# Kernel tuning notes

Measured on AMD Instinct MI355X. Metric: run time of the kernel, lower is better.

The kernel has to match this reference:

```python
import jax, jax.numpy as jnp
import numpy as np

HIDDEN = 1024
NUM_EXPERTS = 64
MIN_K, MAX_K = 1, 4
THRESHOLD = 0.5
N_TOKENS = 32768


def setup_inputs() -> dict:
    key = jax.random.key(0)
    ks = jax.random.split(key, 6)
    std = 0.02
    h4 = HIDDEN // 4
    return {
        "hidden_states": jax.random.normal(ks[0], (N_TOKENS, HIDDEN), dtype=jnp.float32),
        "router_w": std * jax.random.normal(ks[1], (NUM_EXPERTS, HIDDEN), dtype=jnp.float32),
        "w1": std * jax.random.normal(ks[2], (h4, HIDDEN), dtype=jnp.float32),
        "b1": jnp.zeros((h4,), dtype=jnp.float32),
        "w2": std * jax.random.normal(ks[3], (1, h4), dtype=jnp.float32),
        "b2": jnp.zeros((1,), dtype=jnp.float32),
    }


def reference(hidden_states, router_w, w1, b1, w2, b2):
    # complexity predictor: Linear -> ReLU -> Linear -> Sigmoid, squeeze(-1)
    h = jax.nn.relu(hidden_states @ w1.T + b1)                     # [N, H/4]
    complexity = jax.nn.sigmoid(h @ w2.T + b2)[:, 0]               # [N]
    router_logits = hidden_states @ router_w.T                     # [N, E]

    adaptive_k = jnp.where(complexity > THRESHOLD, MAX_K, MIN_K)   # [N] int

    # vectorized adaptive top-k: take MAX_K everywhere, mask beyond k
    top_vals, top_idx = jax.lax.top_k(router_logits, MAX_K)        # [N, MAX_K]
    pos_mask = jnp.arange(MAX_K)[None, :] < adaptive_k[:, None]    # [N, MAX_K]
    masked_vals = jnp.where(pos_mask, top_vals, -jnp.inf)
    expert_weights = jax.nn.softmax(masked_vals, axis=-1)
    expert_weights = jnp.where(pos_mask, expert_weights, 0.0)      # zeros past k
    selected_experts = jnp.where(pos_mask, top_idx, 0)             # zeros past k

    # routing statistics
    probs = jax.nn.softmax(router_logits, axis=-1)                 # [N, E]
    expert_load = probs.mean(axis=0)                               # [E]
    load_variance = expert_load.var(ddof=1)                        # torch .var() is unbiased
    entropy = -(probs * jnp.log(probs + 1e-8)).sum(axis=-1).mean()

    return router_logits, selected_experts, expert_weights, load_variance, entropy
```

## Files before the change

### kernel.cpp

```cpp
#include <hip/hip_runtime.h>
#include <hip/hip_bf16.h>
#include <math.h>

#define NTOK 32768
#define HID  1024
#define NEXP 64
#define H4   256

typedef __attribute__((ext_vector_type(8))) short bf16x8;
typedef __attribute__((ext_vector_type(8))) unsigned short u16x8;
typedef __attribute__((ext_vector_type(4))) float f32x4;

static __device__ __forceinline__ ushort f2bf(float x) {
    unsigned u = __float_as_uint(x);
    unsigned r = (u + 0x7FFFu + ((u >> 16) & 1u)) >> 16;
    return (ushort)r;
}

static __device__ __forceinline__ void split3r(float x, ushort &h, ushort &m, ushort &l) {
    h = f2bf(x);
    const float r1 = x - __uint_as_float(((unsigned)h) << 16);
    m = f2bf(r1);
    const float r2 = r1 - __uint_as_float(((unsigned)m) << 16);
    l = f2bf(r2);
}

#define SWZ(row, us) ((us) ^ (((row) & 7) << 3))

__global__ __launch_bounds__(256) void prep_kernel(
    const float* __restrict__ W1, const float* __restrict__ RW,
    ushort* __restrict__ W1f, ushort* __restrict__ RWf)
{
    if (blockIdx.x < 256) {
        const int id = blockIdx.x * 256 + threadIdx.x;
        const int c  = id >> 8;
        const int k0 = (id & 255) * 4;
        const float4 v = *(const float4*)(W1 + (size_t)c * HID + k0);
        const int p = k0 >> 5, quad = (k0 >> 3) & 3, kk = k0 & 7;
        const int cg = c >> 6, j = (c >> 4) & 3, l15 = c & 15;
        const int lane = quad * 16 + l15;
        const size_t base = (size_t)p * 16384 + cg * 4096 + j * 1024 + lane * 8 + kk;
        const float xs[4] = {v.x, v.y, v.z, v.w};
        ushort hv[4], lv[4];
#pragma unroll
        for (int q = 0; q < 4; q++) {
            const ushort h = f2bf(xs[q]);
            hv[q] = h;
            lv[q] = f2bf(xs[q] - __uint_as_float(((unsigned)h) << 16));
        }
        *(ushort4*)(W1f + base)       = make_ushort4(hv[0], hv[1], hv[2], hv[3]);
        *(ushort4*)(W1f + base + 512) = make_ushort4(lv[0], lv[1], lv[2], lv[3]);
    } else {
        const int e  = blockIdx.x - 256;
        const int k0 = threadIdx.x * 4;
        const float4 v = *(const float4*)(RW + (size_t)e * HID + k0);
        const int p = k0 >> 5, quad = (k0 >> 3) & 3, kk = k0 & 7;
        const int cg = e >> 4, l15 = e & 15;
        const int lane = quad * 16 + l15;
        const size_t base = (size_t)p * 6144 + cg * 1536 + lane * 8 + kk;
        const float xs[4] = {v.x, v.y, v.z, v.w};
        ushort h[4], m[4], l[4];
#pragma unroll
        for (int q = 0; q < 4; q++) split3r(xs[q], h[q], m[q], l[q]);
        *(ushort4*)(RWf + base)        = make_ushort4(h[0], h[1], h[2], h[3]);
        *(ushort4*)(RWf + base + 512)  = make_ushort4(m[0], m[1], m[2], m[3]);
        *(ushort4*)(RWf + base + 1024) = make_ushort4(l[0], l[1], l[2], l[3]);
    }
}

template<int PH>
__device__ __forceinline__ void kstep(
    int p, int cg, int lane, int quad, int l15, int row, int kc,
    const float* __restrict__ xsrc,
    const ushort* __restrict__ RWf, const ushort* __restrict__ W1f,
    ushort (&Xh)[2][2048], ushort (&Xm)[2][2048], ushort (&Xl)[2][2048],
    bf16x8 (&rwh)[2], bf16x8 (&rwm)[2], bf16x8 (&rwl)[2],
    float4 (&xp)[2][2],
    f32x4 (&accL)[4], f32x4 (&accP)[4][4])
{
    const ushort* __restrict__ w1p = W1f + (size_t)p * 16384 + cg * 4096 + lane * 8;
    bf16x8 bwh[4], bwl[4];
#pragma unroll
    for (int j = 0; j < 4; ++j) {
        bwh[j] = *(const bf16x8*)(w1p + j * 1024);
        bwl[j] = *(const bf16x8*)(w1p + j * 1024 + 512);
    }
    {
        const ushort* __restrict__ rwp =
            RWf + (size_t)((p + 1) & 31) * 6144 + cg * 1536 + lane * 8;
        rwh[PH ^ 1] = *(const bf16x8*)(rwp);
        rwm[PH ^ 1] = *(const bf16x8*)(rwp + 512);
        rwl[PH ^ 1] = *(const bf16x8*)(rwp + 1024);
    }
    xp[PH ^ 1][0] = *(const float4*)(xsrc + (size_t)((p + 2) & 31) * 32);
    xp[PH ^ 1][1] = *(const float4*)(xsrc + (size_t)((p + 2) & 31) * 32 + 4);

    bf16x8 axh[4], axm[4], axl[4];
#pragma unroll
    for (int f = 0; f < 4; ++f) {
        const int ra = f * 16 + l15;
        const int ua = SWZ(ra, ra * 32 + quad * 8);
        axh[f] = *(const bf16x8*)&Xh[PH][ua];
        axm[f] = *(const bf16x8*)&Xm[PH][ua];
        axl[f] = *(const bf16x8*)&Xl[PH][ua];
    }

    {
        const float xs[8] = {xp[PH][0].x, xp[PH][0].y, xp[PH][0].z, xp[PH][0].w,
                             xp[PH][1].x, xp[PH][1].y, xp[PH][1].z, xp[PH][1].w};
        u16x8 sh, sm, sl;
#pragma unroll
        for (int q = 0; q < 8; ++q) {
            ushort h, m, l;
            split3r(xs[q], h, m, l);
            sh[q] = h; sm[q] = m; sl[q] = l;
        }
        const int us = SWZ(row, row * 32 + kc * 8);
        *(u16x8*)&Xh[PH ^ 1][us] = sh;
        *(u16x8*)&Xm[PH ^ 1][us] = sm;
        *(u16x8*)&Xl[PH ^ 1][us] = sl;
    }

#pragma unroll
    for (int f = 0; f < 4; ++f) {
        accL[f] = __builtin_amdgcn_mfma_f32_16x16x32_bf16(axh[f], rwh[PH], accL[f], 0, 0, 0);
        accL[f] = __builtin_amdgcn_mfma_f32_16x16x32_bf16(axm[f], rwh[PH], accL[f], 0, 0, 0);
        accL[f] = __builtin_amdgcn_mfma_f32_16x16x32_bf16(axh[f], rwm[PH], accL[f], 0, 0, 0);
        accL[f] = __builtin_amdgcn_mfma_f32_16x16x32_bf16(axl[f], rwh[PH], accL[f], 0, 0, 0);
        accL[f] = __builtin_amdgcn_mfma_f32_16x16x32_bf16(axh[f], rwl[PH], accL[f], 0, 0, 0);
        accL[f] = __builtin_amdgcn_mfma_f32_16x16x32_bf16(axm[f], rwm[PH], accL[f], 0, 0, 0);
    }
#pragma unroll
    for (int j = 0; j < 4; ++j)
#pragma unroll
        for (int f = 0; f < 4; ++f) {
            accP[f][j] = __builtin_amdgcn_mfma_f32_16x16x32_bf16(axh[f], bwh[j], accP[f][j], 0, 0, 0);
            accP[f][j] = __builtin_amdgcn_mfma_f32_16x16x32_bf16(axm[f], bwh[j], accP[f][j], 0, 0, 0);
            accP[f][j] = __builtin_amdgcn_mfma_f32_16x16x32_bf16(axh[f], bwl[j], accP[f][j], 0, 0, 0);
        }

    asm volatile("s_waitcnt lgkmcnt(0)" ::: "memory");
    __builtin_amdgcn_s_barrier();
    __builtin_amdgcn_sched_barrier(0);
}

__global__ __launch_bounds__(256, 2) void fused_mfma(
    const float* __restrict__ X,
    const ushort* __restrict__ RWf, const ushort* __restrict__ W1f,
    const float* __restrict__ B1, const float* __restrict__ W2,
    float* __restrict__ logits, float* __restrict__ s2ws)
{
    __shared__ __align__(16) ushort Xh[2][2048], Xm[2][2048], Xl[2][2048];
    __shared__ float red[4][64];

    const int tid  = threadIdx.x;
    const int lane = tid & 63;
    const int cg   = tid >> 6;
    const int quad = lane >> 4, l15 = lane & 15;
    const int tok0 = blockIdx.x * 64;

    const int row = tid >> 2;
    const int kc  = tid & 3;

    f32x4 accL[4];
    f32x4 accP[4][4];
#pragma unroll
    for (int f = 0; f < 4; f++) {
        accL[f] = (f32x4){0.f, 0.f, 0.f, 0.f};
#pragma unroll
        for (int j = 0; j < 4; j++) accP[f][j] = (f32x4){0.f, 0.f, 0.f, 0.f};
    }

    const float* __restrict__ xsrc = X + (size_t)(tok0 + row) * HID + kc * 8;

    bf16x8 rwh[2], rwm[2], rwl[2];
    float4 xp[2][2];

    {
        const float4 a0 = *(const float4*)(xsrc);
        const float4 a1 = *(const float4*)(xsrc + 4);
        const float xs[8] = {a0.x, a0.y, a0.z, a0.w, a1.x, a1.y, a1.z, a1.w};
        u16x8 sh, sm, sl;
#pragma unroll
        for (int q = 0; q < 8; ++q) {
            ushort h, m, l;
            split3r(xs[q], h, m, l);
            sh[q] = h; sm[q] = m; sl[q] = l;
        }
        const int us = SWZ(row, row * 32 + kc * 8);
        *(u16x8*)&Xh[0][us] = sh;
        *(u16x8*)&Xm[0][us] = sm;
        *(u16x8*)&Xl[0][us] = sl;
    }
    {
        const ushort* __restrict__ rwp = RWf + (size_t)cg * 1536 + lane * 8;
        rwh[0] = *(const bf16x8*)(rwp);
        rwm[0] = *(const bf16x8*)(rwp + 512);
        rwl[0] = *(const bf16x8*)(rwp + 1024);
    }
    xp[0][0] = *(const float4*)(xsrc + 32);
    xp[0][1] = *(const float4*)(xsrc + 36);
    __syncthreads();

    for (int p = 0; p < 32; p += 2) {
        kstep<0>(p,     cg, lane, quad, l15, row, kc, xsrc, RWf, W1f,
                 Xh, Xm, Xl, rwh, rwm, rwl, xp, accL, accP);
        kstep<1>(p + 1, cg, lane, quad, l15, row, kc, xsrc, RWf, W1f,
                 Xh, Xm, Xl, rwh, rwm, rwl, xp, accL, accP);
    }

#pragma unroll
    for (int f = 0; f < 4; ++f)
#pragma unroll
        for (int r = 0; r < 4; ++r)
            logits[(size_t)(tok0 + f * 16 + quad * 4 + r) * NEXP
                   + cg * 16 + l15] = accL[f][r];

    float w2r[4], b1r[4];
#pragma unroll
    for (int j = 0; j < 4; ++j) {
        const int col = (cg * 4 + j) * 16 + l15;
        w2r[j] = W2[col];
        b1r[j] = B1[col];
    }
#pragma unroll
    for (int f = 0; f < 4; ++f) {
#pragma unroll
        for (int r = 0; r < 4; ++r) {
            float s = 0.f;
#pragma unroll
            for (int j = 0; j < 4; ++j) {
                const float hval = accP[f][j][r] + b1r[j];
                s = fmaf(w2r[j], fmaxf(hval, 0.f), s);
            }
            s += __shfl_xor(s, 1);
            s += __shfl_xor(s, 2);
            s += __shfl_xor(s, 4);
            s += __shfl_xor(s, 8);
            if (l15 == 0)
                red[cg][f * 16 + quad * 4 + r] = s;
        }
    }
    __syncthreads();
    if (tid < 64)
        s2ws[tok0 + tid] = red[0][tid] + red[1][tid] + red[2][tid] + red[3][tid];
}

__global__ __launch_bounds__(64) void route_kernel(
    const float* __restrict__ logits, const float* __restrict__ s2ws,
    const float* __restrict__ B2, float* __restrict__ sel,
    float* __restrict__ wts, float* __restrict__ load_sum,
    float* __restrict__ ent_sum)
{
    const int lane = threadIdx.x;
    const int tok  = blockIdx.x * 64 + lane;

    float r[64];
    const float* lr = logits + (size_t)tok * NEXP;
#pragma unroll
    for (int e4 = 0; e4 < 16; e4++) {
        float4 v = *(const float4*)(lr + e4 * 4);
        r[e4 * 4 + 0] = v.x; r[e4 * 4 + 1] = v.y;
        r[e4 * 4 + 2] = v.z; r[e4 * 4 + 3] = v.w;
    }

    float v0 = -1e30f, v1 = -1e30f, v2 = -1e30f, v3 = -1e30f;
    int   i0 = 0, i1 = 0, i2 = 0, i3 = 0;
#pragma unroll
    for (int e = 0; e < 64; e++) {
        const float v = r[e];
        if (v > v3) {
            if (v > v2) {
                if (v > v1) {
                    if (v > v0) { v3=v2;i3=i2; v2=v1;i2=i1; v1=v0;i1=i0; v0=v;i0=e; }
                    else        { v3=v2;i3=i2; v2=v1;i2=i1; v1=v;i1=e; }
                } else          { v3=v2;i3=i2; v2=v;i2=e; }
            } else              { v3=v;i3=e; }
        }
    }

    const float s2 = s2ws[tok] + B2[0];
    const bool k4 = (s2 > 0.f);

    float w0, w1v, w2v, w3v;
    int   s1i, s2i, s3i;
    if (k4) {
        const float e0 = expf(v0 - v0), e1 = expf(v1 - v0);
        const float e2 = expf(v2 - v0), e3 = expf(v3 - v0);
        const float inv4 = 1.f / (e0 + e1 + e2 + e3);
        w0 = e0 * inv4; w1v = e1 * inv4; w2v = e2 * inv4; w3v = e3 * inv4;
        s1i = i1; s2i = i2; s3i = i3;
    } else {
        w0 = 1.f; w1v = 0.f; w2v = 0.f; w3v = 0.f;
        s1i = 0; s2i = 0; s3i = 0;
    }
    {
        float4 sv = {(float)i0, (float)s1i, (float)s2i, (float)s3i};
        float4 wv = {w0, w1v, w2v, w3v};
        *(float4*)(sel + (size_t)tok * 4) = sv;
        *(float4*)(wts + (size_t)tok * 4) = wv;
    }

    const float mx = v0;
    float S = 0.f, pz = 0.f;
#pragma unroll
    for (int e = 0; e < 64; e++) {
        const float z = r[e] - mx;
        const float t = expf(z);
        S += t; pz = fmaf(t, z, pz);
        r[e] = t;
    }
    const float inv = 1.f / S;
    float ent = logf(S) - pz * inv;

    float myload = 0.f;
#pragma unroll
    for (int e = 0; e < 64; e++) {
        float s = r[e] * inv;
        s += __shfl_xor(s, 1);
        s += __shfl_xor(s, 2);
        s += __shfl_xor(s, 4);
        s += __shfl_xor(s, 8);
        s += __shfl_xor(s, 16);
        s += __shfl_xor(s, 32);
        if (lane == e) myload = s;
    }
    atomicAdd(&load_sum[lane], myload);

    ent += __shfl_xor(ent, 1);
    ent += __shfl_xor(ent, 2);
    ent += __shfl_xor(ent, 4);
    ent += __shfl_xor(ent, 8);
    ent += __shfl_xor(ent, 16);
    ent += __shfl_xor(ent, 32);
    if (lane == 0) atomicAdd(ent_sum, ent);
}

__global__ void finalize_kernel(const float* __restrict__ load_sum,
                                const float* __restrict__ ent_sum,
                                float* __restrict__ out_scal)
{
    const int lane = threadIdx.x;
    const float le = load_sum[lane] * (1.f / (float)NTOK);
    float s = le;
#pragma unroll
    for (int o = 32; o >= 1; o >>= 1) s += __shfl_xor(s, o);
    const float mean = s * (1.f / 64.f);
    const float d = le - mean;
    float v = d * d;
#pragma unroll
    for (int o = 32; o >= 1; o >>= 1) v += __shfl_xor(v, o);
    if (lane == 0) {
        out_scal[0] = v * (1.f / 63.f);
        out_scal[1] = ent_sum[0] * (1.f / (float)NTOK);
    }
}

extern "C" void kernel_launch(void* const* d_in, const int* in_sizes, int n_in,
                              void* d_out, int out_size, void* d_ws, size_t ws_size,
                              hipStream_t stream) {
    const float* X  = (const float*)d_in[0];
    const float* RW = (const float*)d_in[1];
    const float* W1 = (const float*)d_in[2];
    const float* B1 = (const float*)d_in[3];
    const float* W2 = (const float*)d_in[4];
    const float* B2 = (const float*)d_in[5];

    float* out    = (float*)d_out;
    float* logits = out;
    float* sel    = out + (size_t)NTOK * NEXP;
    float* wts    = sel + (size_t)NTOK * 4;
    float* scal   = wts + (size_t)NTOK * 4;

    float* s2ws     = (float*)d_ws;
    float* load_sum = s2ws + NTOK;
    float* ent_sum  = load_sum + 64;
    ushort* W1f = (ushort*)(s2ws + NTOK + 256);
    ushort* RWf = W1f + (size_t)32 * 16384;

    hipMemsetAsync(load_sum, 0, 65 * sizeof(float), stream);

    prep_kernel<<<320, 256, 0, stream>>>(W1, RW, W1f, RWf);
    fused_mfma<<<NTOK / 64, 256, 0, stream>>>(X, RWf, W1f, B1, W2, logits, s2ws);
    route_kernel<<<NTOK / 64, 64, 0, stream>>>(logits, s2ws, B2, sel, wts, load_sum, ent_sum);
    finalize_kernel<<<1, 64, 0, stream>>>(load_sum, ent_sum, scal);
}
```

Baseline: 281.0 us.

## Fuse routing into MFMA kernel and double-buffer W1 fragment loads

The separate route_kernel is merged into the fused MFMA kernel. Logits are staged in a padded shared tile and one wave does top-k, softmax weights, entropy and load reduction, which removes a global logits re-read, the s2ws round trip and a launch. W1 fragments are now prefetched one k-step ahead into double-buffered registers, so global load latency overlaps the MFMAs. The extra shared memory (about 16.6KB) and the extra VGPRs for double-buffered bwh/bwl may reduce occupancy under launch_bounds(256,2). The routing tail also runs on only one of the four waves per block.

```diff
diff --git a/kernel.cpp b/kernel.cpp
--- a/kernel.cpp
+++ b/kernel.cpp
@@ -75,22 +75,25 @@
     const ushort* __restrict__ RWf, const ushort* __restrict__ W1f,
     ushort (&Xh)[2][2048], ushort (&Xm)[2][2048], ushort (&Xl)[2][2048],
     bf16x8 (&rwh)[2], bf16x8 (&rwm)[2], bf16x8 (&rwl)[2],
+    bf16x8 (&bwh)[2][4], bf16x8 (&bwl)[2][4],
     float4 (&xp)[2][2],
     f32x4 (&accL)[4], f32x4 (&accP)[4][4])
 {
-    const ushort* __restrict__ w1p = W1f + (size_t)p * 16384 + cg * 4096 + lane * 8;
-    bf16x8 bwh[4], bwl[4];
-#pragma unroll
-    for (int j = 0; j < 4; ++j) {
-        bwh[j] = *(const bf16x8*)(w1p + j * 1024);
-        bwl[j] = *(const bf16x8*)(w1p + j * 1024 + 512);
-    }
     {
         const ushort* __restrict__ rwp =
             RWf + (size_t)((p + 1) & 31) * 6144 + cg * 1536 + lane * 8;
         rwh[PH ^ 1] = *(const bf16x8*)(rwp);
         rwm[PH ^ 1] = *(const bf16x8*)(rwp + 512);
         rwl[PH ^ 1] = *(const bf16x8*)(rwp + 1024);
+    }
+    {
+        const ushort* __restrict__ w1p =
+            W1f + (size_t)((p + 1) & 31) * 16384 + cg * 4096 + lane * 8;
+#pragma unroll
+        for (int j = 0; j < 4; ++j) {
+            bwh[PH ^ 1][j] = *(const bf16x8*)(w1p + j * 1024);
+            bwl[PH ^ 1][j] = *(const bf16x8*)(w1p + j * 1024 + 512);
+        }
     }
     xp[PH ^ 1][0] = *(const float4*)(xsrc + (size_t)((p + 2) & 31) * 32);
     xp[PH ^ 1][1] = *(const float4*)(xsrc + (size_t)((p + 2) & 31) * 32 + 4);
@@ -134,9 +137,9 @@
     for (int j = 0; j < 4; ++j)
 #pragma unroll
         for (int f = 0; f < 4; ++f) {
-            accP[f][j] = __builtin_amdgcn_mfma_f32_16x16x32_bf16(axh[f], bwh[j], accP[f][j], 0, 0, 0);
-            accP[f][j] = __builtin_amdgcn_mfma_f32_16x16x32_bf16(axm[f], bwh[j], accP[f][j], 0, 0, 0);
-            accP[f][j] = __builtin_amdgcn_mfma_f32_16x16x32_bf16(axh[f], bwl[j], accP[f][j], 0, 0, 0);
+            accP[f][j] = __builtin_amdgcn_mfma_f32_16x16x32_bf16(axh[f], bwh[PH][j], accP[f][j], 0, 0, 0);
+            accP[f][j] = __builtin_amdgcn_mfma_f32_16x16x32_bf16(axm[f], bwh[PH][j], accP[f][j], 0, 0, 0);
+            accP[f][j] = __builtin_amdgcn_mfma_f32_16x16x32_bf16(axh[f], bwl[PH][j], accP[f][j], 0, 0, 0);
         }
 
     asm volatile("s_waitcnt lgkmcnt(0)" ::: "memory");
@@ -148,10 +151,14 @@
     const float* __restrict__ X,
     const ushort* __restrict__ RWf, const ushort* __restrict__ W1f,
     const float* __restrict__ B1, const float* __restrict__ W2,
-    float* __restrict__ logits, float* __restrict__ s2ws)
+    const float* __restrict__ B2,
+    float* __restrict__ logits, float* __restrict__ sel,
+    float* __restrict__ wts, float* __restrict__ load_sum,
+    float* __restrict__ ent_sum)
 {
     __shared__ __align__(16) ushort Xh[2][2048], Xm[2][2048], Xl[2][2048];
     __shared__ float red[4][64];
+    __shared__ float Lt[64][65];
 
     const int tid  = threadIdx.x;
     const int lane = tid & 63;
@@ -174,6 +181,7 @@
     const float* __restrict__ xsrc = X + (size_t)(tok0 + row) * HID + kc * 8;
 
     bf16x8 rwh[2], rwm[2], rwl[2];
+    bf16x8 bwh[2][4], bwl[2][4];
     float4 xp[2][2];
 
     {
@@ -197,6 +205,12 @@
         rwh[0] = *(const bf16x8*)(rwp);
         rwm[0] = *(const bf16x8*)(rwp + 512);
         rwl[0] = *(const bf16x8*)(rwp + 1024);
+        const ushort* __restrict__ w1p = W1f + (size_t)cg * 4096 + lane * 8;
+#pragma unroll
+        for (int j = 0; j < 4; ++j) {
+            bwh[0][j] = *(const bf16x8*)(w1p + j * 1024);
+            bwl[0][j] = *(const bf16x8*)(w1p + j * 1024 + 512);
+        }
     }
     xp[0][0] = *(const float4*)(xsrc + 32);
     xp[0][1] = *(const float4*)(xsrc + 36);
@@ -204,17 +218,19 @@
 
     for (int p = 0; p < 32; p += 2) {
         kstep<0>(p,     cg, lane, quad, l15, row, kc, xsrc, RWf, W1f,
-                 Xh, Xm, Xl, rwh, rwm, rwl, xp, accL, accP);
+                 Xh, Xm, Xl, rwh, rwm, rwl, bwh, bwl, xp, accL, accP);
         kstep<1>(p + 1, cg, lane, quad, l15, row, kc, xsrc, RWf, W1f,
-                 Xh, Xm, Xl, rwh, rwm, rwl, xp, accL, accP);
+                 Xh, Xm, Xl, rwh, rwm, rwl, bwh, bwl, xp, accL, accP);
     }
 
 #pragma unroll
     for (int f = 0; f < 4; ++f)
 #pragma unroll
-        for (int r = 0; r < 4; ++r)
-            logits[(size_t)(tok0 + f * 16 + quad * 4 + r) * NEXP
-                   + cg * 16 + l15] = accL[f][r];
+        for (int r = 0; r < 4; ++r) {
+            const int trow = f * 16 + quad * 4 + r;
+            logits[(size_t)(tok0 + trow) * NEXP + cg * 16 + l15] = accL[f][r];
+            Lt[trow][cg * 16 + l15] = accL[f][r];
+        }
 
     float w2r[4], b1r[4];
 #pragma unroll
@@ -242,98 +258,86 @@
         }
     }
     __syncthreads();
-    if (tid < 64)
-        s2ws[tok0 + tid] = red[0][tid] + red[1][tid] + red[2][tid] + red[3][tid];
-}
-
-__global__ __launch_bounds__(64) void route_kernel(
-    const float* __restrict__ logits, const float* __restrict__ s2ws,
-    const float* __restrict__ B2, float* __restrict__ sel,
-    float* __restrict__ wts, float* __restrict__ load_sum,
-    float* __restrict__ ent_sum)
-{
-    const int lane = threadIdx.x;
-    const int tok  = blockIdx.x * 64 + lane;
-
-    float r[64];
-    const float* lr = logits + (size_t)tok * NEXP;
-#pragma unroll
-    for (int e4 = 0; e4 < 16; e4++) {
-        float4 v = *(const float4*)(lr + e4 * 4);
-        r[e4 * 4 + 0] = v.x; r[e4 * 4 + 1] = v.y;
-        r[e4 * 4 + 2] = v.z; r[e4 * 4 + 3] = v.w;
-    }
-
-    float v0 = -1e30f, v1 = -1e30f, v2 = -1e30f, v3 = -1e30f;
-    int   i0 = 0, i1 = 0, i2 = 0, i3 = 0;
-#pragma unroll
-    for (int e = 0; e < 64; e++) {
-        const float v = r[e];
-        if (v > v3) {
-            if (v > v2) {
-                if (v > v1) {
-                    if (v > v0) { v3=v2;i3=i2; v2=v1;i2=i1; v1=v0;i1=i0; v0=v;i0=e; }
-                    else        { v3=v2;i3=i2; v2=v1;i2=i1; v1=v;i1=e; }
-                } else          { v3=v2;i3=i2; v2=v;i2=e; }
-            } else              { v3=v;i3=e; }
-        }
-    }
-
-    const float s2 = s2ws[tok] + B2[0];
-    const bool k4 = (s2 > 0.f);
-
-    float w0, w1v, w2v, w3v;
-    int   s1i, s2i, s3i;
-    if (k4) {
-        const float e0 = expf(v0 - v0), e1 = expf(v1 - v0);
-        const float e2 = expf(v2 - v0), e3 = expf(v3 - v0);
-        const float inv4 = 1.f / (e0 + e1 + e2 + e3);
-        w0 = e0 * inv4; w1v = e1 * inv4; w2v = e2 * inv4; w3v = e3 * inv4;
-        s1i = i1; s2i = i2; s3i = i3;
-    } else {
-        w0 = 1.f; w1v = 0.f; w2v = 0.f; w3v = 0.f;
-        s1i = 0; s2i = 0; s3i = 0;
-    }
-    {
-        float4 sv = {(float)i0, (float)s1i, (float)s2i, (float)s3i};
-        float4 wv = {w0, w1v, w2v, w3v};
-        *(float4*)(sel + (size_t)tok * 4) = sv;
-        *(float4*)(wts + (size_t)tok * 4) = wv;
-    }
-
-    const float mx = v0;
-    float S = 0.f, pz = 0.f;
-#pragma unroll
-    for (int e = 0; e < 64; e++) {
-        const float z = r[e] - mx;
-        const float t = expf(z);
-        S += t; pz = fmaf(t, z, pz);
-        r[e] = t;
-    }
-    const float inv = 1.f / S;
-    float ent = logf(S) - pz * inv;
-
-    float myload = 0.f;
-#pragma unroll
-    for (int e = 0; e < 64; e++) {
-        float s = r[e] * inv;
-        s += __shfl_xor(s, 1);
-        s += __shfl_xor(s, 2);
-        s += __shfl_xor(s, 4);
-        s += __shfl_xor(s, 8);
-        s += __shfl_xor(s, 16);
-        s += __shfl_xor(s, 32);
-        if (lane == e) myload = s;
-    }
-    atomicAdd(&load_sum[lane], myload);
-
-    ent += __shfl_xor(ent, 1);
-    ent += __shfl_xor(ent, 2);
-    ent += __shfl_xor(ent, 4);
-    ent += __shfl_xor(ent, 8);
-    ent += __shfl_xor(ent, 16);
-    ent += __shfl_xor(ent, 32);
-    if (lane == 0) atomicAdd(ent_sum, ent);
+
+    if (cg == 0) {
+        const int tok = tok0 + lane;
+
+        float r[64];
+#pragma unroll
+        for (int e = 0; e < 64; e++) r[e] = Lt[lane][e];
+
+        float v0 = -1e30f, v1 = -1e30f, v2 = -1e30f, v3 = -1e30f;
+        int   i0 = 0, i1 = 0, i2 = 0, i3 = 0;
+#pragma unroll
+        for (int e = 0; e < 64; e++) {
+            const float v = r[e];
+            if (v > v3) {
+                if (v > v2) {
+                    if (v > v1) {
+                        if (v > v0) { v3=v2;i3=i2; v2=v1;i2=i1; v1=v0;i1=i0; v0=v;i0=e; }
+                        else        { v3=v2;i3=i2; v2=v1;i2=i1; v1=v;i1=e; }
+                    } else          { v3=v2;i3=i2; v2=v;i2=e; }
+                } else              { v3=v;i3=e; }
+            }
+        }
+
+        const float s2 = red[0][lane] + red[1][lane] + red[2][lane]
+                       + red[3][lane] + B2[0];
+        const bool k4 = (s2 > 0.f);
+
+        float w0, w1v, w2v, w3v;
+        int   s1i, s2i, s3i;
+        if (k4) {
+            const float e0 = expf(v0 - v0), e1 = expf(v1 - v0);
+            const float e2 = expf(v2 - v0), e3 = expf(v3 - v0);
+            const float inv4 = 1.f / (e0 + e1 + e2 + e3);
+            w0 = e0 * inv4; w1v = e1 * inv4; w2v = e2 * inv4; w3v = e3 * inv4;
+            s1i = i1; s2i = i2; s3i = i3;
+        } else {
+            w0 = 1.f; w1v = 0.f; w2v = 0.f; w3v = 0.f;
+            s1i = 0; s2i = 0; s3i = 0;
+        }
+        {
+            float4 sv = {(float)i0, (float)s1i, (float)s2i, (float)s3i};
+            float4 wv = {w0, w1v, w2v, w3v};
+            *(float4*)(sel + (size_t)tok * 4) = sv;
+            *(float4*)(wts + (size_t)tok * 4) = wv;
+        }
+
+        const float mx = v0;
+        float S = 0.f, pz = 0.f;
+#pragma unroll
+        for (int e = 0; e < 64; e++) {
+            const float z = r[e] - mx;
+            const float t = expf(z);
+            S += t; pz = fmaf(t, z, pz);
+            r[e] = t;
+        }
+        const float inv = 1.f / S;
+        float ent = logf(S) - pz * inv;
+
+        float myload = 0.f;
+#pragma unroll
+        for (int e = 0; e < 64; e++) {
+            float s = r[e] * inv;
+            s += __shfl_xor(s, 1);
+            s += __shfl_xor(s, 2);
+            s += __shfl_xor(s, 4);
+            s += __shfl_xor(s, 8);
+            s += __shfl_xor(s, 16);
+            s += __shfl_xor(s, 32);
+            if (lane == e) myload = s;
+        }
+        atomicAdd(&load_sum[lane], myload);
+
+        ent += __shfl_xor(ent, 1);
+        ent += __shfl_xor(ent, 2);
+        ent += __shfl_xor(ent, 4);
+        ent += __shfl_xor(ent, 8);
+        ent += __shfl_xor(ent, 16);
+        ent += __shfl_xor(ent, 32);
+        if (lane == 0) atomicAdd(ent_sum, ent);
+    }
 }
 
 __global__ void finalize_kernel(const float* __restrict__ load_sum,
@@ -381,7 +385,7 @@
     hipMemsetAsync(load_sum, 0, 65 * sizeof(float), stream);
 
     prep_kernel<<<320, 256, 0, stream>>>(W1, RW, W1f, RWf);
-    fused_mfma<<<NTOK / 64, 256, 0, stream>>>(X, RWf, W1f, B1, W2, logits, s2ws);
-    route_kernel<<<NTOK / 64, 64, 0, stream>>>(logits, s2ws, B2, sel, wts, load_sum, ent_sum);
+    fused_mfma<<<NTOK / 64, 256, 0, stream>>>(X, RWf, W1f, B1, W2, B2,
+                                              logits, sel, wts, load_sum, ent_sum);
     finalize_kernel<<<1, 64, 0, stream>>>(load_sum, ent_sum, scal);
 }
```

New measurement: 254.7 us. -9.3%, faster.
